# Kernel tuning notes

Hardware: AMD Instinct MI355X
Metric: run time of the kernel (lower is better)

Reference implementation:

```python
import jax, jax.numpy as jnp
import numpy as np

N, C, H, K, HID = 131072, 256, 8, 128, 1024
SCALE = (C // H) ** -0.5  # 1/sqrt(32)


def layernorm(x, g, b, eps=1e-5):
    mu = jnp.mean(x, axis=-1, keepdims=True)
    var = jnp.var(x, axis=-1, keepdims=True)
    return (x - mu) * jax.lax.rsqrt(var + eps) * g + b


def setup_inputs() -> dict:
    key = jax.random.key(0)
    ks = jax.random.split(key, 8)
    feat = jax.random.normal(ks[0], (N, C), dtype=jnp.float32)
    order = jax.random.permutation(ks[1], N)  # serialized order (gather)
    inverse = jnp.argsort(order)              # scatter back (unpad identity)
    s = 0.02
    return {
        "feat": feat,
        "ln1_g": jnp.ones((C,), jnp.float32), "ln1_b": jnp.zeros((C,), jnp.float32),
        "w_qkv": jax.random.normal(ks[2], (C, 3 * C), jnp.float32) * s,
        "b_qkv": jnp.zeros((3 * C,), jnp.float32),
        "w_proj": jax.random.normal(ks[3], (C, C), jnp.float32) * s,
        "b_proj": jnp.zeros((C,), jnp.float32),
        "ln2_g": jnp.ones((C,), jnp.float32), "ln2_b": jnp.zeros((C,), jnp.float32),
        "w1": jax.random.normal(ks[4], (C, HID), jnp.float32) * s,
        "b1": jnp.zeros((HID,), jnp.float32),
        "w2": jax.random.normal(ks[5], (HID, C), jnp.float32) * s,
        "b2": jnp.zeros((C,), jnp.float32),
        "order": order,
        "inverse": inverse,
    }


def attention(x, w_qkv, b_qkv, w_proj, b_proj, order, inverse):
    D = C // H
    qkv = x @ w_qkv + b_qkv                       # [N, 3C]
    qkv = qkv[order]                              # gather to serialized order
    qkv = qkv.reshape(-1, K, 3, H, D)             # [P, K, 3, H, D]
    q, k, v = jnp.moveaxis(qkv, 2, 0)             # each [P, K, H, D]
    q = jnp.swapaxes(q, 1, 2)                     # [P, H, K, D]
    k = jnp.swapaxes(k, 1, 2)
    v = jnp.swapaxes(v, 1, 2)
    attn = jnp.einsum("phkd,phjd->phkj", q * SCALE, k)  # [P, H, K, K]
    attn = jax.nn.softmax(attn, axis=-1)
    out = jnp.einsum("phkj,phjd->phkd", attn, v)  # [P, H, K, D]
    out = jnp.swapaxes(out, 1, 2).reshape(-1, C)  # [N, C]
    out = out[inverse]                            # scatter back to input order
    return out @ w_proj + b_proj


def reference(feat, ln1_g, ln1_b, w_qkv, b_qkv, w_proj, b_proj,
              ln2_g, ln2_b, w1, b1, w2, b2, order, inverse):
    # pre-norm transformer block: x + attn(ln1(x)); x + mlp(ln2(x))
    x = feat
    x = x + attention(layernorm(x, ln1_g, ln1_b), w_qkv, b_qkv, w_proj, b_proj, order, inverse)
    h = layernorm(x, ln2_g, ln2_b)
    h = jax.nn.gelu(h @ w1 + b1) @ w2 + b2
    return x + h
```

## Files before the change

### kernel.cpp

```cpp
#include <hip/hip_runtime.h>
#include <hip/hip_bf16.h>

typedef __hip_bfloat16 bf16;
typedef __bf16 bf16x8 __attribute__((ext_vector_type(8)));
typedef float f32x4 __attribute__((ext_vector_type(4)));

#define N_TOK 131072
#define C_DIM 256
#define HID_DIM 1024

__device__ __forceinline__ void async_copy16(void* lds, const void* g) {
  __builtin_amdgcn_global_load_lds(
      (const __attribute__((address_space(1))) void*)g,
      (__attribute__((address_space(3))) void*)lds, 16, 0, 0);
}

__device__ __forceinline__ float fast_gelu(float x) {
  float y = 0.7978845608028654f * (x + 0.044715f * x * x * x);
  float e = __expf(2.f * y);
  float th = 1.f - 2.f / (e + 1.f);
  return 0.5f * x * (1.f + th);
}

__global__ void ln_bf16_kernel(const float* __restrict__ x,
                               const float* __restrict__ g,
                               const float* __restrict__ b,
                               bf16* __restrict__ out) {
  int row = blockIdx.x * 4 + threadIdx.y;
  int lane = threadIdx.x;
  size_t base = (size_t)row * C_DIM + lane * 4;
  float4 v = *(const float4*)(x + base);
  float s = v.x + v.y + v.z + v.w;
  float s2 = v.x * v.x + v.y * v.y + v.z * v.z + v.w * v.w;
#pragma unroll
  for (int m = 1; m < 64; m <<= 1) { s += __shfl_xor(s, m); s2 += __shfl_xor(s2, m); }
  float mean = s * (1.f / 256.f);
  float var = s2 * (1.f / 256.f) - mean * mean;
  float rstd = rsqrtf(var + 1e-5f);
  float4 gv = *(const float4*)(g + lane * 4);
  float4 bv = *(const float4*)(b + lane * 4);
  union { bf16 h[4]; uint2 u; } pk;
  pk.h[0] = __float2bfloat16((v.x - mean) * rstd * gv.x + bv.x);
  pk.h[1] = __float2bfloat16((v.y - mean) * rstd * gv.y + bv.y);
  pk.h[2] = __float2bfloat16((v.z - mean) * rstd * gv.z + bv.z);
  pk.h[3] = __float2bfloat16((v.w - mean) * rstd * gv.w + bv.w);
  *(uint2*)(out + base) = pk.u;
}

__global__ void cast_transpose_kernel(const float* __restrict__ in, bf16* __restrict__ out,
                                      int K, int N) {
  int idx = blockIdx.x * 256 + threadIdx.x;
  if (idx >= K * N) return;
  int n = idx / K, k = idx - n * K;
  out[idx] = __float2bfloat16(in[(size_t)k * N + n]);
}

template <int EPI>
__global__ __launch_bounds__(256) void gemm_bt_kernel(
    const bf16* __restrict__ A, const bf16* __restrict__ Bt,
    const float* __restrict__ bias, const float* __restrict__ res,
    void* __restrict__ outp, int K, int ldn) {
  __shared__ bf16 sA[128 * 64];
  __shared__ bf16 sB[128 * 64];
  const int tid = threadIdx.x;
  const int wid = tid >> 6;
  const int lane = tid & 63;
  const int quad = lane >> 4;
  const int l16 = lane & 15;
  const int m0 = blockIdx.x * 128;
  const int n0 = blockIdx.y * 128;
  const int wm = (wid >> 1) * 64;
  const int wn = (wid & 1) * 64;
  const int srow = tid >> 3;
  const int scol = (tid & 7) * 8;

  f32x4 acc[4][4] = {};

  for (int k0 = 0; k0 < K; k0 += 64) {
#pragma unroll
    for (int is = 0; is < 4; ++is) {
      async_copy16(&sA[is * 2048 + wid * 512],
                   &A[(size_t)(m0 + is * 32 + srow) * K + k0 + scol]);
      async_copy16(&sB[is * 2048 + wid * 512],
                   &Bt[(size_t)(n0 + is * 32 + srow) * K + k0 + scol]);
    }
    __syncthreads();
#pragma unroll
    for (int kk = 0; kk < 64; kk += 32) {
      bf16x8 af[4], bfr[4];
#pragma unroll
      for (int i = 0; i < 4; ++i)
        af[i] = *(const bf16x8*)&sA[(wm + i * 16 + l16) * 64 + kk + quad * 8];
#pragma unroll
      for (int j = 0; j < 4; ++j)
        bfr[j] = *(const bf16x8*)&sB[(wn + j * 16 + l16) * 64 + kk + quad * 8];
#pragma unroll
      for (int i = 0; i < 4; ++i)
#pragma unroll
        for (int j = 0; j < 4; ++j)
          acc[i][j] = __builtin_amdgcn_mfma_f32_16x16x32_bf16(af[i], bfr[j], acc[i][j], 0, 0, 0);
    }
    __syncthreads();
  }

#pragma unroll
  for (int i = 0; i < 4; ++i) {
    int rowb = m0 + wm + i * 16 + quad * 4;
#pragma unroll
    for (int j = 0; j < 4; ++j) {
      int col = n0 + wn + j * 16 + l16;
      float bv = bias[col];
#pragma unroll
      for (int r = 0; r < 4; ++r) {
        size_t idx = (size_t)(rowb + r) * ldn + col;
        float v = acc[i][j][r] + bv;
        if constexpr (EPI == 0) {
          ((bf16*)outp)[idx] = __float2bfloat16(v);
        } else if constexpr (EPI == 1) {
          ((float*)outp)[idx] = v + res[idx];
        } else if constexpr (EPI == 2) {
          ((bf16*)outp)[idx] = __float2bfloat16(fast_gelu(v));
        } else {
          ((float*)outp)[idx] = v + res[idx];
        }
      }
    }
  }
}

__global__ __launch_bounds__(256) void attn_kernel(
    const bf16* __restrict__ qkv, const int* __restrict__ order,
    bf16* __restrict__ outw) {
  __shared__ bf16 sK[128 * 40];
  __shared__ bf16 sVt[32 * 136];
  __shared__ bf16 sP[128 * 136];
  __shared__ int sOrd[128];
  const int p = blockIdx.x;
  const int h = blockIdx.y;
  const int tid = threadIdx.x;
  const int wid = tid >> 6;
  const int lane = tid & 63;
  const int quad = lane >> 4;
  const int l16 = lane & 15;

  if (tid < 128) sOrd[tid] = order[p * 128 + tid];
  __syncthreads();

  {
    int r = tid >> 1;
    int half = (tid & 1) * 16;
    size_t base = (size_t)sOrd[r] * 768 + h * 32;
    uint4 ka = *(const uint4*)&qkv[base + 256 + half];
    uint4 kb = *(const uint4*)&qkv[base + 256 + half + 8];
    *(uint4*)&sK[r * 40 + half] = ka;
    *(uint4*)&sK[r * 40 + half + 8] = kb;
    union { uint4 u[2]; bf16 e[16]; } vv;
    vv.u[0] = *(const uint4*)&qkv[base + 512 + half];
    vv.u[1] = *(const uint4*)&qkv[base + 512 + half + 8];
#pragma unroll
    for (int c = 0; c < 16; ++c) sVt[(half + c) * 136 + r] = vv.e[c];
  }
  __syncthreads();

  bf16x8 qf[2];
#pragma unroll
  for (int t = 0; t < 2; ++t) {
    int r = wid * 32 + t * 16 + l16;
    qf[t] = *(const bf16x8*)&qkv[(size_t)sOrd[r] * 768 + h * 32 + quad * 8];
  }

  const f32x4 zero = {0.f, 0.f, 0.f, 0.f};
  f32x4 s[2][8];
#pragma unroll
  for (int ct = 0; ct < 8; ++ct) {
    bf16x8 kf = *(const bf16x8*)&sK[(ct * 16 + l16) * 40 + quad * 8];
#pragma unroll
    for (int t = 0; t < 2; ++t)
      s[t][ct] = __builtin_amdgcn_mfma_f32_16x16x32_bf16(qf[t], kf, zero, 0, 0, 0);
  }

  const float scale = 0.17677669529663687f;
#pragma unroll
  for (int t = 0; t < 2; ++t) {
#pragma unroll
    for (int r = 0; r < 4; ++r) {
      float mx = -1e30f;
#pragma unroll
      for (int ct = 0; ct < 8; ++ct) mx = fmaxf(mx, s[t][ct][r]);
      mx *= scale;
#pragma unroll
      for (int mk = 1; mk < 16; mk <<= 1) mx = fmaxf(mx, __shfl_xor(mx, mk));
      float sum = 0.f;
#pragma unroll
      for (int ct = 0; ct < 8; ++ct) {
        float e = __expf(scale * s[t][ct][r] - mx);
        s[t][ct][r] = e;
        sum += e;
      }
#pragma unroll
      for (int mk = 1; mk < 16; mk <<= 1) sum += __shfl_xor(sum, mk);
      float inv = 1.f / sum;
      int prow = wid * 32 + t * 16 + quad * 4 + r;
#pragma unroll
      for (int ct = 0; ct < 8; ++ct)
        sP[prow * 136 + ct * 16 + l16] = __float2bfloat16(s[t][ct][r] * inv);
    }
  }
  __syncthreads();

  f32x4 o[2][2] = {};
#pragma unroll
  for (int ks = 0; ks < 4; ++ks) {
    bf16x8 vf[2];
#pragma unroll
    for (int n = 0; n < 2; ++n)
      vf[n] = *(const bf16x8*)&sVt[(n * 16 + l16) * 136 + ks * 32 + quad * 8];
#pragma unroll
    for (int t = 0; t < 2; ++t) {
      bf16x8 pf = *(const bf16x8*)&sP[(wid * 32 + t * 16 + l16) * 136 + ks * 32 + quad * 8];
#pragma unroll
      for (int n = 0; n < 2; ++n)
        o[t][n] = __builtin_amdgcn_mfma_f32_16x16x32_bf16(pf, vf[n], o[t][n], 0, 0, 0);
    }
  }

#pragma unroll
  for (int t = 0; t < 2; ++t) {
    int rowb = wid * 32 + t * 16 + quad * 4;
#pragma unroll
    for (int r = 0; r < 4; ++r) {
      size_t gbase = (size_t)sOrd[rowb + r] * 256 + h * 32;
#pragma unroll
      for (int n = 0; n < 2; ++n)
        outw[gbase + n * 16 + l16] = __float2bfloat16(o[t][n][r]);
    }
  }
}

extern "C" void kernel_launch(void* const* d_in, const int* in_sizes, int n_in,
                              void* d_out, int out_size, void* d_ws, size_t ws_size,
                              hipStream_t stream) {
  const float* feat   = (const float*)d_in[0];
  const float* ln1_g  = (const float*)d_in[1];
  const float* ln1_b  = (const float*)d_in[2];
  const float* w_qkv  = (const float*)d_in[3];
  const float* b_qkv  = (const float*)d_in[4];
  const float* w_proj = (const float*)d_in[5];
  const float* b_proj = (const float*)d_in[6];
  const float* ln2_g  = (const float*)d_in[7];
  const float* ln2_b  = (const float*)d_in[8];
  const float* w1     = (const float*)d_in[9];
  const float* b1     = (const float*)d_in[10];
  const float* w2     = (const float*)d_in[11];
  const float* b2     = (const float*)d_in[12];
  const int* order    = (const int*)d_in[13];
  float* out = (float*)d_out;

  char* ws = (char*)d_ws;
  size_t off = 0;
  auto take = [&](size_t bytes) {
    char* pp = ws + off;
    off += (bytes + 255) & ~(size_t)255;
    return pp;
  };
  bf16* ln_buf  = (bf16*)take((size_t)N_TOK * 256 * 2);
  bf16* qkv     = (bf16*)take((size_t)N_TOK * 768 * 2);
  bf16* attn_o  = (bf16*)take((size_t)N_TOK * 256 * 2);
  float* xres   = (float*)take((size_t)N_TOK * 256 * 4);
  bf16* wqkvT   = (bf16*)take(768 * 256 * 2);
  bf16* wprojT  = (bf16*)take(256 * 256 * 2);
  bf16* w1T     = (bf16*)take(1024 * 256 * 2);
  bf16* w2T     = (bf16*)take(256 * 1024 * 2);
  bf16* hbuf    = qkv;

  cast_transpose_kernel<<<768, 256, 0, stream>>>(w_qkv, wqkvT, 256, 768);
  cast_transpose_kernel<<<256, 256, 0, stream>>>(w_proj, wprojT, 256, 256);
  cast_transpose_kernel<<<1024, 256, 0, stream>>>(w1, w1T, 256, 1024);
  cast_transpose_kernel<<<1024, 256, 0, stream>>>(w2, w2T, 1024, 256);

  ln_bf16_kernel<<<N_TOK / 4, dim3(64, 4), 0, stream>>>(feat, ln1_g, ln1_b, ln_buf);
  gemm_bt_kernel<0><<<dim3(1024, 6), 256, 0, stream>>>(ln_buf, wqkvT, b_qkv, nullptr, qkv, 256, 768);
  attn_kernel<<<dim3(1024, 8), 256, 0, stream>>>(qkv, order, attn_o);
  gemm_bt_kernel<1><<<dim3(1024, 2), 256, 0, stream>>>(attn_o, wprojT, b_proj, feat, xres, 256, 256);
  ln_bf16_kernel<<<N_TOK / 4, dim3(64, 4), 0, stream>>>(xres, ln2_g, ln2_b, ln_buf);
  gemm_bt_kernel<2><<<dim3(1024, 8), 256, 0, stream>>>(ln_buf, w1T, b1, nullptr, hbuf, 256, 1024);
  gemm_bt_kernel<3><<<dim3(1024, 2), 256, 0, stream>>>(hbuf, w2T, b2, xres, out, 1024, 256);
}
```

Baseline: 972.9 us.

## Swizzle GEMM LDS layout, swap grid order, use fast reciprocal

Applies an XOR swizzle to the LDS column index in the GEMM tiles so MFMA fragment reads avoid bank conflicts. It also swaps the grid dimensions of the GEMM and attention kernels so blocks sharing the same A rows or tokens run next to each other, which improves L2 reuse. Smaller edits hoist bias loads and pointer arithmetic and replace divisions in GELU and softmax with a hardware reciprocal. The reciprocal is slightly less accurate than a true division.

```diff
diff --git a/kernel.cpp b/kernel.cpp
--- a/kernel.cpp
+++ b/kernel.cpp
@@ -15,10 +15,18 @@
       (__attribute__((address_space(3))) void*)lds, 16, 0, 0);
 }
 
+__device__ __forceinline__ float fast_rcp(float x) {
+#if __has_builtin(__builtin_amdgcn_rcpf)
+  return __builtin_amdgcn_rcpf(x);
+#else
+  return 1.f / x;
+#endif
+}
+
 __device__ __forceinline__ float fast_gelu(float x) {
-  float y = 0.7978845608028654f * (x + 0.044715f * x * x * x);
+  float y = 0.7978845608028654f * x * (1.f + 0.044715f * x * x);
   float e = __expf(2.f * y);
-  float th = 1.f - 2.f / (e + 1.f);
+  float th = 1.f - 2.f * fast_rcp(e + 1.f);
   return 0.5f * x * (1.f + th);
 }
 
@@ -67,33 +75,39 @@
   const int lane = tid & 63;
   const int quad = lane >> 4;
   const int l16 = lane & 15;
-  const int m0 = blockIdx.x * 128;
-  const int n0 = blockIdx.y * 128;
+  const int n0 = blockIdx.x * 128;
+  const int m0 = blockIdx.y * 128;
   const int wm = (wid >> 1) * 64;
   const int wn = (wid & 1) * 64;
   const int srow = tid >> 3;
-  const int scol = (tid & 7) * 8;
+  const int scol = ((tid & 7) ^ (srow & 7)) * 8;
+
+  const bf16* pA = A + (size_t)(m0 + srow) * K + scol;
+  const bf16* pB = Bt + (size_t)(n0 + srow) * K + scol;
+  const size_t isStride = (size_t)32 * K;
 
   f32x4 acc[4][4] = {};
 
   for (int k0 = 0; k0 < K; k0 += 64) {
 #pragma unroll
     for (int is = 0; is < 4; ++is) {
-      async_copy16(&sA[is * 2048 + wid * 512],
-                   &A[(size_t)(m0 + is * 32 + srow) * K + k0 + scol]);
-      async_copy16(&sB[is * 2048 + wid * 512],
-                   &Bt[(size_t)(n0 + is * 32 + srow) * K + k0 + scol]);
-    }
+      async_copy16(&sA[is * 2048 + wid * 512], pA + is * isStride);
+      async_copy16(&sB[is * 2048 + wid * 512], pB + is * isStride);
+    }
+    pA += 64;
+    pB += 64;
     __syncthreads();
 #pragma unroll
     for (int kk = 0; kk < 64; kk += 32) {
       bf16x8 af[4], bfr[4];
 #pragma unroll
       for (int i = 0; i < 4; ++i)
-        af[i] = *(const bf16x8*)&sA[(wm + i * 16 + l16) * 64 + kk + quad * 8];
+        af[i] = *(const bf16x8*)&sA[(wm + i * 16 + l16) * 64 +
+                                    ((((kk >> 3) + quad) ^ (l16 & 7)) << 3)];
 #pragma unroll
       for (int j = 0; j < 4; ++j)
-        bfr[j] = *(const bf16x8*)&sB[(wn + j * 16 + l16) * 64 + kk + quad * 8];
+        bfr[j] = *(const bf16x8*)&sB[(wn + j * 16 + l16) * 64 +
+                                     ((((kk >> 3) + quad) ^ (l16 & 7)) << 3)];
 #pragma unroll
       for (int i = 0; i < 4; ++i)
 #pragma unroll
@@ -103,17 +117,20 @@
     __syncthreads();
   }
 
+  float bv[4];
+#pragma unroll
+  for (int j = 0; j < 4; ++j) bv[j] = bias[n0 + wn + j * 16 + l16];
+  const int colb = n0 + wn + l16;
 #pragma unroll
   for (int i = 0; i < 4; ++i) {
     int rowb = m0 + wm + i * 16 + quad * 4;
 #pragma unroll
-    for (int j = 0; j < 4; ++j) {
-      int col = n0 + wn + j * 16 + l16;
-      float bv = bias[col];
-#pragma unroll
-      for (int r = 0; r < 4; ++r) {
-        size_t idx = (size_t)(rowb + r) * ldn + col;
-        float v = acc[i][j][r] + bv;
+    for (int r = 0; r < 4; ++r) {
+      size_t rowoff = (size_t)(rowb + r) * ldn + colb;
+#pragma unroll
+      for (int j = 0; j < 4; ++j) {
+        size_t idx = rowoff + j * 16;
+        float v = acc[i][j][r] + bv[j];
         if constexpr (EPI == 0) {
           ((bf16*)outp)[idx] = __float2bfloat16(v);
         } else if constexpr (EPI == 1) {
@@ -135,8 +152,8 @@
   __shared__ bf16 sVt[32 * 136];
   __shared__ bf16 sP[128 * 136];
   __shared__ int sOrd[128];
-  const int p = blockIdx.x;
-  const int h = blockIdx.y;
+  const int h = blockIdx.x;
+  const int p = blockIdx.y;
   const int tid = threadIdx.x;
   const int wid = tid >> 6;
   const int lane = tid & 63;
@@ -199,7 +216,7 @@
       }
 #pragma unroll
       for (int mk = 1; mk < 16; mk <<= 1) sum += __shfl_xor(sum, mk);
-      float inv = 1.f / sum;
+      float inv = fast_rcp(sum);
       int prow = wid * 32 + t * 16 + quad * 4 + r;
 #pragma unroll
       for (int ct = 0; ct < 8; ++ct)
@@ -279,10 +296,10 @@
   cast_transpose_kernel<<<1024, 256, 0, stream>>>(w2, w2T, 1024, 256);
 
   ln_bf16_kernel<<<N_TOK / 4, dim3(64, 4), 0, stream>>>(feat, ln1_g, ln1_b, ln_buf);
-  gemm_bt_kernel<0><<<dim3(1024, 6), 256, 0, stream>>>(ln_buf, wqkvT, b_qkv, nullptr, qkv, 256, 768);
-  attn_kernel<<<dim3(1024, 8), 256, 0, stream>>>(qkv, order, attn_o);
-  gemm_bt_kernel<1><<<dim3(1024, 2), 256, 0, stream>>>(attn_o, wprojT, b_proj, feat, xres, 256, 256);
+  gemm_bt_kernel<0><<<dim3(6, 1024), 256, 0, stream>>>(ln_buf, wqkvT, b_qkv, nullptr, qkv, 256, 768);
+  attn_kernel<<<dim3(8, 1024), 256, 0, stream>>>(qkv, order, attn_o);
+  gemm_bt_kernel<1><<<dim3(2, 1024), 256, 0, stream>>>(attn_o, wprojT, b_proj, feat, xres, 256, 256);
   ln_bf16_kernel<<<N_TOK / 4, dim3(64, 4), 0, stream>>>(xres, ln2_g, ln2_b, ln_buf);
-  gemm_bt_kernel<2><<<dim3(1024, 8), 256, 0, stream>>>(ln_buf, w1T, b1, nullptr, hbuf, 256, 1024);
-  gemm_bt_kernel<3><<<dim3(1024, 2), 256, 0, stream>>>(hbuf, w2T, b2, xres, out, 1024, 256);
-}
+  gemm_bt_kernel<2><<<dim3(8, 1024), 256, 0, stream>>>(ln_buf, w1T, b1, nullptr, hbuf, 256, 1024);
+  gemm_bt_kernel<3><<<dim3(2, 1024), 256, 0, stream>>>(hbuf, w2T, b2, xres, out, 1024, 256);
+}
```

Result: faster. 868.3 us (-10.8%).
